# Kernel optimization log

Hardware: AMD Instinct MI355X
Metric: run time of the kernel (lower is better)

Reference implementation:

```python
import jax, jax.numpy as jnp
import numpy as np

D_MODEL = 1024
NEG_INF = -1e30


def _xavier(key, shape):
    fan_in, fan_out = shape[0], shape[1] if len(shape) > 1 else shape[0]
    limit = float(np.sqrt(6.0 / (fan_in + fan_out)))
    return jax.random.uniform(key, shape, jnp.float32, -limit, limit)


def setup_inputs() -> dict:
    key = jax.random.key(0)
    ks = jax.random.split(key, 8)
    bs, vl, ql, d = 16, 1024, 64, D_MODEL
    video_features = jax.random.normal(ks[0], (bs, vl, d), jnp.float32)
    query_features = jax.random.normal(ks[1], (bs, ql, d), jnp.float32)
    video_mask = jnp.ones((bs, vl), jnp.float32)
    query_mask = jnp.ones((bs, ql), jnp.float32)
    sim_w = _xavier(ks[2], (d, 1))
    cor_v_w = _xavier(ks[3], (1, d))
    cor_q_w = _xavier(ks[4], (1, 1))
    pool_w = _xavier(ks[5], (d, 1))          # WeightedPool weight
    mixer_w = _xavier(ks[6], (4 * d, d))     # 1x1 conv == dense mix
    mixer_b = jnp.zeros((d,), jnp.float32)
    return dict(video_features=video_features, query_features=query_features,
                video_mask=video_mask, query_mask=query_mask,
                sim_w=sim_w, cor_v_w=cor_v_w, cor_q_w=cor_q_w,
                pool_w=pool_w, mixer_w=mixer_w, mixer_b=mixer_b)


def reference(video_features, query_features, video_mask, query_mask,
              sim_w, cor_v_w, cor_q_w, pool_w, mixer_w, mixer_b):
    bs, vl, d = video_features.shape
    ql = query_features.shape[1]
    # correlation: (q_exp * v_exp).sum(-1) is just a batched matmul -> (bs, ql, vl)
    corr = jnp.einsum('bqd,bvd->bqv', query_features, video_features)
    scores = jax.nn.softmax(corr, axis=1)  # softmax over query dim (torch dim=1)
    # cor_w[b,q,d] = cor_v_w[0,d] * cor_q_w[0,0]; corr_matrix = scores^T @ cor_w
    cor_w = jnp.broadcast_to(cor_v_w * cor_q_w[0, 0], (ql, d))
    corr_matrix = jnp.einsum('bqv,qd->bvd', scores, cor_w)
    # WeightedPool over query words -> sentence feature (bs, d)
    alpha = jnp.einsum('bqd,dk->bqk', query_features, pool_w)[..., 0]  # (bs, ql)
    alpha = alpha + (1.0 - query_mask) * NEG_INF
    alphas = jax.nn.softmax(alpha, axis=1)
    sentence = jnp.einsum('bqd,bq->bd', query_features, alphas)  # (bs, d)
    # cosine similarity video vs sentence (+ masked log)
    eps = 1e-8
    dot = jnp.einsum('bvd,bd->bv', video_features, sentence)
    vn = jnp.maximum(jnp.linalg.norm(video_features, axis=-1), eps)
    sn = jnp.maximum(jnp.linalg.norm(sentence, axis=-1), eps)
    sim = dot / (vn * sn[:, None]) + jnp.log(video_mask + 1e-45)  # (bs, vl)
    # sim_features[b,v,d] = sim_w[d,0] * sim[b,v]
    sim_features = sim[..., None] * sim_w[:, 0]
    pooled_query = jnp.broadcast_to(sentence[:, None, :], (bs, vl, d))
    features = jnp.concatenate([video_features, sim_features, pooled_query, corr_matrix], axis=2)
    out = jnp.einsum('bvc,cd->bvd', features, mixer_w) + mixer_b
    return jax.nn.relu(out)
```

## Files before the change

### kernel.cpp

```cpp
#include <hip/hip_runtime.h>

#define BS 16
#define VL 1024
#define QL 64
#define DM 1024
#define MM (BS*VL)

typedef __attribute__((ext_vector_type(8))) short bf16x8;
typedef __attribute__((ext_vector_type(4))) float f32x4;

__device__ __forceinline__ unsigned short f2bf_rne(float f) {
  unsigned int u = __float_as_uint(f);
  u += 0x7fffu + ((u >> 16) & 1u);
  return (unsigned short)(u >> 16);
}
__device__ __forceinline__ void gl16(const void* g, void* l) {
  __builtin_amdgcn_global_load_lds(
      (const __attribute__((address_space(1))) unsigned int*)g,
      (__attribute__((address_space(3))) unsigned int*)l, 16, 0, 0);
}

__global__ __launch_bounds__(256) void k_sentence(
    const float* __restrict__ query, const float* __restrict__ qmask,
    const float* __restrict__ pool_w, float* __restrict__ sentence,
    float* __restrict__ sn)
{
  int b = blockIdx.x, t = threadIdx.x;
  __shared__ float alpha[QL];
  __shared__ float red[4];
  const float* qb = query + (size_t)b*QL*DM;
  {
    int q = t >> 2, part = t & 3;
    const float4* rp = (const float4*)(qb + q*DM + part*256);
    const float4* pp = (const float4*)(pool_w + part*256);
    float s = 0.f;
    for (int i = 0; i < 64; ++i) {
      float4 a = rp[i], w = pp[i];
      s += a.x*w.x + a.y*w.y + a.z*w.z + a.w*w.w;
    }
    s += __shfl_xor(s, 1);
    s += __shfl_xor(s, 2);
    if (part == 0) alpha[q] = s;
  }
  __syncthreads();
  if (t < 64) {
    float a = alpha[t] + (1.f - qmask[b*QL + t]) * (-1e30f);
    float m = a;
    for (int off = 32; off; off >>= 1) m = fmaxf(m, __shfl_xor(m, off));
    float e = expf(a - m);
    float ssum = e;
    for (int off = 32; off; off >>= 1) ssum += __shfl_xor(ssum, off);
    alpha[t] = e / ssum;
  }
  __syncthreads();
  float sq = 0.f;
  #pragma unroll
  for (int i = 0; i < 4; ++i) {
    int d = t + 256*i;
    float acc = 0.f;
    for (int q = 0; q < QL; ++q) acc += alpha[q] * qb[q*DM + d];
    sentence[(size_t)b*DM + d] = acc;
    sq += acc*acc;
  }
  for (int off = 32; off; off >>= 1) sq += __shfl_xor(sq, off);
  if ((t & 63) == 0) red[t >> 6] = sq;
  __syncthreads();
  if (t == 0) sn[b] = fmaxf(sqrtf(red[0]+red[1]+red[2]+red[3]), 1e-8f);
}

__global__ __launch_bounds__(256) void k_gemvs(
    const float* __restrict__ mixer_w, const float* __restrict__ sentence,
    const float* __restrict__ sim_w, const float* __restrict__ cor_v_w,
    const float* __restrict__ cor_q_w, float* __restrict__ partial)
{
  int d0 = blockIdx.x * 32;
  int n0 = blockIdx.y * 128;
  int t = threadIdx.x;
  int col = t & 127, kh = t >> 7;
  __shared__ float vec[18][32];
  __shared__ float red[2][18][128];
  for (int i = t; i < 18*32; i += 256) {
    int b = i >> 5, k = i & 31;
    float val;
    if (b < 16)       val = sentence[(size_t)b*DM + d0 + k];
    else if (b == 16) val = sim_w[d0 + k];
    else              val = cor_v_w[d0 + k] * cor_q_w[0];
    vec[b][k] = val;
  }
  __syncthreads();
  float acc[18];
  #pragma unroll
  for (int j = 0; j < 18; ++j) acc[j] = 0.f;
  const float* Wb = mixer_w + (size_t)(d0 + kh*16)*DM + n0 + col;
  #pragma unroll 1
  for (int k = 0; k < 16; ++k) {
    const float* wr = Wb + (size_t)k*DM;
    float w1 = wr[(size_t)1*DM*DM];
    float w2 = wr[(size_t)2*DM*DM];
    float w3 = wr[(size_t)3*DM*DM];
    int kk = kh*16 + k;
    #pragma unroll
    for (int b = 0; b < 16; ++b) acc[b] += vec[b][kk] * w2;
    acc[16] += vec[16][kk] * w1;
    acc[17] += vec[17][kk] * w3;
  }
  #pragma unroll
  for (int j = 0; j < 18; ++j) red[kh][j][col] = acc[j];
  __syncthreads();
  #pragma unroll
  for (int r = 0; r < 9; ++r) {
    int idx = t + 256*r;
    int j = idx >> 7, c2 = idx & 127;
    partial[((size_t)blockIdx.x*18 + j)*1024 + n0 + c2] = red[0][j][c2] + red[1][j][c2];
  }
}

__global__ __launch_bounds__(256) void k_reduce(
    const float* __restrict__ partial, float* __restrict__ basev,
    float* __restrict__ u_s, float* __restrict__ u_c)
{
  int idx = blockIdx.x * 256 + threadIdx.x;
  int j = idx >> 10, col = idx & 1023;
  float s = 0.f;
  #pragma unroll 4
  for (int b = 0; b < 32; ++b) s += partial[((size_t)b*18 + j)*1024 + col];
  if (j < 16)       basev[(size_t)j*1024 + col] = s;
  else if (j == 16) u_s[col] = s;
  else              u_c[col] = s;
}

__global__ __launch_bounds__(256) void k_conv(
    const float* __restrict__ video, const float* __restrict__ sentence,
    const float* __restrict__ sn, const float* __restrict__ vmask,
    const float* __restrict__ Wv,
    unsigned short* __restrict__ Ahi, unsigned short* __restrict__ Bhi,
    float* __restrict__ simv)
{
  __shared__ float tile[64][65];
  int t = threadIdx.x;
  if (blockIdx.x < 4096) {
    int wave = t >> 6, lane = t & 63;
    int row = blockIdx.x * 4 + wave;
    int b = row >> 10;
    const float4* vp = (const float4*)(video + (size_t)row*DM);
    const float4* sp = (const float4*)(sentence + (size_t)b*DM);
    float dot = 0.f, sq = 0.f;
    #pragma unroll
    for (int i = 0; i < 4; ++i) {
      float4 v = vp[lane + 64*i];
      float4 s = sp[lane + 64*i];
      dot += v.x*s.x + v.y*s.y + v.z*s.z + v.w*s.w;
      sq  += v.x*v.x + v.y*v.y + v.z*v.z + v.w*v.w;
      ushort4 h;
      h.x = f2bf_rne(v.x); h.y = f2bf_rne(v.y);
      h.z = f2bf_rne(v.z); h.w = f2bf_rne(v.w);
      *(ushort4*)(Ahi + (size_t)row*DM + (lane + 64*i)*4) = h;
    }
    #pragma unroll
    for (int off = 32; off; off >>= 1) {
      dot += __shfl_xor(dot, off);
      sq  += __shfl_xor(sq,  off);
    }
    if (lane == 0) {
      float vn = fmaxf(sqrtf(sq), 1e-8f);
      simv[row] = dot / (vn * sn[b]) + logf(vmask[row] + 1e-45f);
    }
  } else {
    int bb = blockIdx.x - 4096;
    int bk = (bb & 15) * 64;
    int bn = (bb >> 4) * 64;
    int kr = t >> 2, nc = (t & 3) * 16;
    const float4* src = (const float4*)(Wv + (size_t)(bk + kr)*DM + bn + nc);
    #pragma unroll
    for (int i = 0; i < 4; ++i) {
      float4 v = src[i];
      tile[kr][nc + i*4 + 0] = v.x;
      tile[kr][nc + i*4 + 1] = v.y;
      tile[kr][nc + i*4 + 2] = v.z;
      tile[kr][nc + i*4 + 3] = v.w;
    }
    __syncthreads();
    int n = t >> 2, kc = (t & 3) * 16;
    #pragma unroll
    for (int i = 0; i < 16; i += 4) {
      ushort4 h;
      h.x = f2bf_rne(tile[kc+i+0][n]);
      h.y = f2bf_rne(tile[kc+i+1][n]);
      h.z = f2bf_rne(tile[kc+i+2][n]);
      h.w = f2bf_rne(tile[kc+i+3][n]);
      *(ushort4*)(Bhi + (size_t)(bn+n)*DM + bk + kc + i) = h;
    }
  }
}

__global__ __launch_bounds__(256) void k_gemm(
    const unsigned short* __restrict__ Ahi, const unsigned short* __restrict__ Bhi,
    const float* __restrict__ simv, const float* __restrict__ u_s,
    const float* __restrict__ u_c, const float* __restrict__ basev,
    const float* __restrict__ mixer_b, float* __restrict__ out)
{
  __shared__ __align__(16) unsigned short At[2][128][64];
  __shared__ __align__(16) unsigned short Bt[2][128][64];

  int bid = blockIdx.x;
  int swz = (bid & 7) * 128 + (bid >> 3);
  int bm = swz >> 3;
  int bn = swz & 7;

  int t = threadIdx.x;
  int wave = t >> 6, lane = t & 63;
  int wm = (wave >> 1) * 64, wn = (wave & 1) * 64;
  int lr = lane & 15, g = lane >> 4;
  int rx = 8 * (lr & 7);

  f32x4 acc[4][4];
  #pragma unroll
  for (int i = 0; i < 4; ++i)
    #pragma unroll
    for (int j = 0; j < 4; ++j) acc[i][j] = (f32x4){0.f, 0.f, 0.f, 0.f};

  int srow = t >> 3;
  int scol = 8 * ((t & 7) ^ (srow & 7));
  const unsigned short* Ap = Ahi + (size_t)(bm*128 + srow)*DM + scol;
  const unsigned short* Bp = Bhi + (size_t)(bn*128 + srow)*DM + scol;
  char* ldsA = (char*)&At[0][0][0] + wave*1024;
  char* ldsB = (char*)&Bt[0][0][0] + wave*1024;

  #define STAGE(kt, buf) do {                                         \
    const unsigned short* _a = Ap + (kt)*64;                          \
    const unsigned short* _b = Bp + (kt)*64;                          \
    _Pragma("unroll")                                                 \
    for (int q = 0; q < 4; ++q) {                                     \
      gl16(_a + (size_t)q*32*DM, ldsA + (buf)*16384 + q*4096);        \
      gl16(_b + (size_t)q*32*DM, ldsB + (buf)*16384 + q*4096);        \
    }                                                                 \
  } while (0)

  STAGE(0, 0);
  __syncthreads();

  #pragma unroll 1
  for (int kt = 0; kt < 16; ++kt) {
    int buf = kt & 1;
    if (kt < 15) STAGE(kt + 1, buf ^ 1);
    const unsigned short* Ab = &At[buf][0][0];
    const unsigned short* Bb = &Bt[buf][0][0];
    #pragma unroll
    for (int s = 0; s < 2; ++s) {
      int cb = (s*32 + 8*g) ^ rx;
      bf16x8 af[4], bfr[4];
      #pragma unroll
      for (int mi = 0; mi < 4; ++mi)
        af[mi] = *(const bf16x8*)(Ab + (wm + mi*16 + lr)*64 + cb);
      #pragma unroll
      for (int nj = 0; nj < 4; ++nj)
        bfr[nj] = *(const bf16x8*)(Bb + (wn + nj*16 + lr)*64 + cb);
      #pragma unroll
      for (int mi = 0; mi < 4; ++mi)
        #pragma unroll
        for (int nj = 0; nj < 4; ++nj)
          acc[mi][nj] = __builtin_amdgcn_mfma_f32_16x16x32_bf16(
              af[mi], bfr[nj], acc[mi][nj], 0, 0, 0);
    }
    __syncthreads();
  }

  int orow0 = bm*128 + wm;
  int ocol0 = bn*128 + wn;
  const float* bb = basev + (size_t)((bm*128) >> 10)*DM;
  float usv[4], cv[4];
  #pragma unroll
  for (int nj = 0; nj < 4; ++nj) {
    int col = ocol0 + nj*16 + lr;
    usv[nj] = u_s[col];
    cv[nj]  = bb[col] + u_c[col] + mixer_b[col];
  }
  int rbase = g * 4;
  #pragma unroll
  for (int mi = 0; mi < 4; ++mi) {
    #pragma unroll
    for (int r = 0; r < 4; ++r) {
      int row = orow0 + mi*16 + rbase + r;
      float sim = simv[row];
      #pragma unroll
      for (int nj = 0; nj < 4; ++nj) {
        float v = acc[mi][nj][r] + sim*usv[nj] + cv[nj];
        out[(size_t)row*DM + ocol0 + nj*16 + lr] = fmaxf(v, 0.f);
      }
    }
  }
  #undef STAGE
}

extern "C" void kernel_launch(void* const* d_in, const int* in_sizes, int n_in,
                              void* d_out, int out_size, void* d_ws, size_t ws_size,
                              hipStream_t stream) {
  const float* video   = (const float*)d_in[0];
  const float* query   = (const float*)d_in[1];
  const float* vmask   = (const float*)d_in[2];
  const float* qmask   = (const float*)d_in[3];
  const float* sim_w   = (const float*)d_in[4];
  const float* cor_v_w = (const float*)d_in[5];
  const float* cor_q_w = (const float*)d_in[6];
  const float* pool_w  = (const float*)d_in[7];
  const float* mixer_w = (const float*)d_in[8];
  const float* mixer_b = (const float*)d_in[9];
  float* out = (float*)d_out;

  float* fws      = (float*)d_ws;
  float* sentence = fws;
  float* sn       = sentence + 16384;
  float* u_s      = sn + 64;
  float* u_c      = u_s + 1024;
  float* basev    = u_c + 1024;
  float* simv     = basev + 16384;
  float* partial  = simv + 16384;
  unsigned short* Ahi = (unsigned short*)(partial + 589824);
  unsigned short* Bhi = Ahi + (size_t)MM*DM;

  k_sentence<<<dim3(16), dim3(256), 0, stream>>>(query, qmask, pool_w, sentence, sn);
  k_conv<<<dim3(4352), dim3(256), 0, stream>>>(video, sentence, sn, vmask,
                                               mixer_w, Ahi, Bhi, simv);
  k_gemvs<<<dim3(32, 8), dim3(256), 0, stream>>>(mixer_w, sentence, sim_w,
                                                 cor_v_w, cor_q_w, partial);
  k_reduce<<<dim3(72), dim3(256), 0, stream>>>(partial, basev, u_s, u_c);
  k_gemm<<<dim3(1024), dim3(256), 0, stream>>>(Ahi, Bhi, simv, u_s, u_c,
                                               basev, mixer_b, out);
}
```

Measured before the change: 220.7 us.

## Enlarge GEMM tile to 256x256 with phased ping-pong schedule and parallelize sentence pooling

The main GEMM moves from 128x128 tiles with 4 waves to 256x256 tiles with 8 waves. Each k-step is split into four phases that interleave LDS fragment reads, MFMA bursts raised with s_setprio, and staggered global-to-LDS prefetches, with explicit vmcnt waits and barriers. This raises operand reuse and overlaps loads with compute. Separately, the single-block-per-batch sentence kernel is split into a 256-block alpha GEMV and a 16x8-grid pooling kernel that writes partial squared norms, which k_conv then sums. Costs are higher register pressure, 64KB of LDS, fewer GEMM blocks (256) for the available CUs, and a fragile hand-written wait/barrier schedule.

```diff
diff --git a/kernel.cpp b/kernel.cpp
--- a/kernel.cpp
+++ b/kernel.cpp
@@ -20,52 +20,64 @@
       (__attribute__((address_space(3))) unsigned int*)l, 16, 0, 0);
 }
 
-__global__ __launch_bounds__(256) void k_sentence(
+__global__ __launch_bounds__(256) void k_alpha(
+    const float* __restrict__ query, const float* __restrict__ pool_w,
+    float* __restrict__ alpha_raw)
+{
+  int wave = threadIdx.x >> 6, lane = threadIdx.x & 63;
+  int q = blockIdx.x * 4 + wave;
+  const float4* rp = (const float4*)(query + (size_t)q*DM);
+  const float4* pp = (const float4*)pool_w;
+  float s = 0.f;
+  #pragma unroll
+  for (int i = 0; i < 4; ++i) {
+    float4 a = rp[lane + 64*i], w = pp[lane + 64*i];
+    s += a.x*w.x + a.y*w.y + a.z*w.z + a.w*w.w;
+  }
+  #pragma unroll
+  for (int off = 32; off; off >>= 1) s += __shfl_xor(s, off);
+  if (lane == 0) alpha_raw[q] = s;
+}
+
+__global__ __launch_bounds__(256) void k_sentence2(
     const float* __restrict__ query, const float* __restrict__ qmask,
-    const float* __restrict__ pool_w, float* __restrict__ sentence,
-    float* __restrict__ sn)
-{
-  int b = blockIdx.x, t = threadIdx.x;
-  __shared__ float alpha[QL];
-  __shared__ float red[4];
-  const float* qb = query + (size_t)b*QL*DM;
-  {
-    int q = t >> 2, part = t & 3;
-    const float4* rp = (const float4*)(qb + q*DM + part*256);
-    const float4* pp = (const float4*)(pool_w + part*256);
-    float s = 0.f;
-    for (int i = 0; i < 64; ++i) {
-      float4 a = rp[i], w = pp[i];
-      s += a.x*w.x + a.y*w.y + a.z*w.z + a.w*w.w;
-    }
-    s += __shfl_xor(s, 1);
-    s += __shfl_xor(s, 2);
-    if (part == 0) alpha[q] = s;
-  }
-  __syncthreads();
+    const float* __restrict__ alpha_raw, float* __restrict__ sentence,
+    float* __restrict__ psq)
+{
+  int b = blockIdx.x, dc = blockIdx.y;
+  int t = threadIdx.x;
+  __shared__ float al[QL];
+  __shared__ float red2[2][128];
+  __shared__ float sqred[2];
   if (t < 64) {
-    float a = alpha[t] + (1.f - qmask[b*QL + t]) * (-1e30f);
+    float a = alpha_raw[b*QL + t] + (1.f - qmask[b*QL + t]) * (-1e30f);
     float m = a;
+    #pragma unroll
     for (int off = 32; off; off >>= 1) m = fmaxf(m, __shfl_xor(m, off));
     float e = expf(a - m);
-    float ssum = e;
-    for (int off = 32; off; off >>= 1) ssum += __shfl_xor(ssum, off);
-    alpha[t] = e / ssum;
-  }
-  __syncthreads();
-  float sq = 0.f;
-  #pragma unroll
-  for (int i = 0; i < 4; ++i) {
-    int d = t + 256*i;
-    float acc = 0.f;
-    for (int q = 0; q < QL; ++q) acc += alpha[q] * qb[q*DM + d];
-    sentence[(size_t)b*DM + d] = acc;
-    sq += acc*acc;
-  }
-  for (int off = 32; off; off >>= 1) sq += __shfl_xor(sq, off);
-  if ((t & 63) == 0) red[t >> 6] = sq;
-  __syncthreads();
-  if (t == 0) sn[b] = fmaxf(sqrtf(red[0]+red[1]+red[2]+red[3]), 1e-8f);
+    float s = e;
+    #pragma unroll
+    for (int off = 32; off; off >>= 1) s += __shfl_xor(s, off);
+    al[t] = e / s;
+  }
+  __syncthreads();
+  int col = t & 127, half = t >> 7;
+  const float* qb = query + (size_t)b*QL*DM + dc*128 + col;
+  float acc = 0.f;
+  for (int q = half*32; q < half*32 + 32; ++q)
+    acc += al[q] * qb[(size_t)q*DM];
+  red2[half][col] = acc;
+  __syncthreads();
+  if (t < 128) {
+    float s = red2[0][t] + red2[1][t];
+    sentence[(size_t)b*DM + dc*128 + t] = s;
+    float sq = s*s;
+    #pragma unroll
+    for (int off = 32; off; off >>= 1) sq += __shfl_xor(sq, off);
+    if ((t & 63) == 0) sqred[t >> 6] = sq;
+  }
+  __syncthreads();
+  if (t == 0) psq[b*8 + dc] = sqred[0] + sqred[1];
 }
 
 __global__ __launch_bounds__(256) void k_gemvs(
@@ -131,7 +143,7 @@
 
 __global__ __launch_bounds__(256) void k_conv(
     const float* __restrict__ video, const float* __restrict__ sentence,
-    const float* __restrict__ sn, const float* __restrict__ vmask,
+    const float* __restrict__ psq, const float* __restrict__ vmask,
     const float* __restrict__ Wv,
     unsigned short* __restrict__ Ahi, unsigned short* __restrict__ Bhi,
     float* __restrict__ simv)
@@ -162,8 +174,12 @@
       sq  += __shfl_xor(sq,  off);
     }
     if (lane == 0) {
-      float vn = fmaxf(sqrtf(sq), 1e-8f);
-      simv[row] = dot / (vn * sn[b]) + logf(vmask[row] + 1e-45f);
+      float ss = 0.f;
+      #pragma unroll
+      for (int i = 0; i < 8; ++i) ss += psq[b*8 + i];
+      float snv = fmaxf(sqrtf(ss), 1e-8f);
+      float vn  = fmaxf(sqrtf(sq), 1e-8f);
+      simv[row] = dot / (vn * snv) + logf(vmask[row] + 1e-45f);
     }
   } else {
     int bb = blockIdx.x - 4096;
@@ -193,81 +209,117 @@
   }
 }
 
-__global__ __launch_bounds__(256) void k_gemm(
+__global__ __launch_bounds__(512, 2) void k_gemm(
     const unsigned short* __restrict__ Ahi, const unsigned short* __restrict__ Bhi,
     const float* __restrict__ simv, const float* __restrict__ u_s,
     const float* __restrict__ u_c, const float* __restrict__ basev,
     const float* __restrict__ mixer_b, float* __restrict__ out)
 {
-  __shared__ __align__(16) unsigned short At[2][128][64];
-  __shared__ __align__(16) unsigned short Bt[2][128][64];
+  __shared__ __align__(16) unsigned short A_lds[2][256][64];
+  __shared__ __align__(16) unsigned short B_lds[2][256][64];
 
   int bid = blockIdx.x;
-  int swz = (bid & 7) * 128 + (bid >> 3);
-  int bm = swz >> 3;
-  int bn = swz & 7;
+  int swz = (bid & 7) * 32 + (bid >> 3);
+  int bm = swz >> 2;
+  int bn = swz & 3;
 
   int t = threadIdx.x;
-  int wave = t >> 6, lane = t & 63;
-  int wm = (wave >> 1) * 64, wn = (wave & 1) * 64;
+  int w = t >> 6, lane = t & 63;
+  int wmh = w >> 2;
+  int wq  = w & 3;
   int lr = lane & 15, g = lane >> 4;
   int rx = 8 * (lr & 7);
 
-  f32x4 acc[4][4];
-  #pragma unroll
-  for (int i = 0; i < 4; ++i)
+  int rsub = lane >> 3, cch = lane & 7;
+  int csw = 8 * (cch ^ rsub);
+  const unsigned short* Asrc =
+      Ahi + (size_t)(bm*256 + wmh*128 + wq*32 + rsub)*DM + csw;
+  const unsigned short* Bsrc =
+      Bhi + (size_t)(bn*256 + wq*64 + wmh*32 + rsub)*DM + csw;
+
+  f32x4 acc[8][4];
+  #pragma unroll
+  for (int i = 0; i < 8; ++i)
     #pragma unroll
     for (int j = 0; j < 4; ++j) acc[i][j] = (f32x4){0.f, 0.f, 0.f, 0.f};
 
-  int srow = t >> 3;
-  int scol = 8 * ((t & 7) ^ (srow & 7));
-  const unsigned short* Ap = Ahi + (size_t)(bm*128 + srow)*DM + scol;
-  const unsigned short* Bp = Bhi + (size_t)(bn*128 + srow)*DM + scol;
-  char* ldsA = (char*)&At[0][0][0] + wave*1024;
-  char* ldsB = (char*)&Bt[0][0][0] + wave*1024;
-
-  #define STAGE(kt, buf) do {                                         \
-    const unsigned short* _a = Ap + (kt)*64;                          \
-    const unsigned short* _b = Bp + (kt)*64;                          \
-    _Pragma("unroll")                                                 \
-    for (int q = 0; q < 4; ++q) {                                     \
-      gl16(_a + (size_t)q*32*DM, ldsA + (buf)*16384 + q*4096);        \
-      gl16(_b + (size_t)q*32*DM, ldsB + (buf)*16384 + q*4096);        \
-    }                                                                 \
-  } while (0)
-
-  STAGE(0, 0);
-  __syncthreads();
+  bf16x8 a_frag[8];
+  bf16x8 b_frag[4];
+
+#define PH_READS_A(h)                                                      \
+  _Pragma("unroll") for (int m = 0; m < 4; ++m)                            \
+    _Pragma("unroll") for (int ks = 0; ks < 2; ++ks)                       \
+      a_frag[m*2+ks] = *(const bf16x8*)                                    \
+          &A_lds[buf][wmh*128 + ((h)*4+m)*16 + lr][(ks*32 + 8*g) ^ rx];
+
+#define PH_READS_B(v)                                                      \
+  _Pragma("unroll") for (int n = 0; n < 2; ++n)                            \
+    _Pragma("unroll") for (int ks = 0; ks < 2; ++ks)                       \
+      b_frag[n*2+ks] = *(const bf16x8*)                                    \
+          &B_lds[buf][wq*64 + ((v)*2+n)*16 + lr][(ks*32 + 8*g) ^ rx];
+
+#define PH_MFMA(h, v)                                                      \
+  __builtin_amdgcn_s_setprio(1);                                           \
+  _Pragma("unroll") for (int m = 0; m < 4; ++m)                            \
+    _Pragma("unroll") for (int n = 0; n < 2; ++n)                          \
+      _Pragma("unroll") for (int ks = 0; ks < 2; ++ks)                     \
+        acc[(h)*4+m][(v)*2+n] = __builtin_amdgcn_mfma_f32_16x16x32_bf16(   \
+            a_frag[m*2+ks], b_frag[n*2+ks], acc[(h)*4+m][(v)*2+n], 0,0,0); \
+  __builtin_amdgcn_s_setprio(0);
+
+  {
+    unsigned short* Ad = &A_lds[0][wmh*128 + wq*32][0];
+    unsigned short* Bd = &B_lds[0][wq*64 + wmh*32][0];
+    #pragma unroll
+    for (int j = 0; j < 4; ++j) {
+      gl16(Asrc + (size_t)j*8*DM, Ad + j*8*64);
+      gl16(Bsrc + (size_t)j*8*DM, Bd + j*8*64);
+    }
+  }
 
   #pragma unroll 1
   for (int kt = 0; kt < 16; ++kt) {
     int buf = kt & 1;
-    if (kt < 15) STAGE(kt + 1, buf ^ 1);
-    const unsigned short* Ab = &At[buf][0][0];
-    const unsigned short* Bb = &Bt[buf][0][0];
-    #pragma unroll
-    for (int s = 0; s < 2; ++s) {
-      int cb = (s*32 + 8*g) ^ rx;
-      bf16x8 af[4], bfr[4];
-      #pragma unroll
-      for (int mi = 0; mi < 4; ++mi)
-        af[mi] = *(const bf16x8*)(Ab + (wm + mi*16 + lr)*64 + cb);
-      #pragma unroll
-      for (int nj = 0; nj < 4; ++nj)
-        bfr[nj] = *(const bf16x8*)(Bb + (wn + nj*16 + lr)*64 + cb);
-      #pragma unroll
-      for (int mi = 0; mi < 4; ++mi)
-        #pragma unroll
-        for (int nj = 0; nj < 4; ++nj)
-          acc[mi][nj] = __builtin_amdgcn_mfma_f32_16x16x32_bf16(
-              af[mi], bfr[nj], acc[mi][nj], 0, 0, 0);
-    }
-    __syncthreads();
-  }
-
-  int orow0 = bm*128 + wm;
-  int ocol0 = bn*128 + wn;
-  const float* bb = basev + (size_t)((bm*128) >> 10)*DM;
+    const unsigned short* An = Asrc + (kt+1)*64;
+    const unsigned short* Bn = Bsrc + (kt+1)*64;
+    unsigned short* Ad = &A_lds[buf^1][wmh*128 + wq*32][0];
+    unsigned short* Bd = &B_lds[buf^1][wq*64 + wmh*32][0];
+    bool pf = kt < 15;
+
+    if (pf) { gl16(An, Ad); gl16(An + (size_t)8*DM, Ad + 8*64); }
+    if (pf) asm volatile("s_waitcnt vmcnt(2)" ::: "memory");
+    else    asm volatile("s_waitcnt vmcnt(0)" ::: "memory");
+    __builtin_amdgcn_sched_barrier(0);
+    __builtin_amdgcn_s_barrier();
+    PH_READS_A(0)
+    PH_READS_B(0)
+    __builtin_amdgcn_s_barrier();
+    PH_MFMA(0, 0)
+    __builtin_amdgcn_s_barrier();
+
+    if (pf) { gl16(An + (size_t)16*DM, Ad + 16*64); gl16(An + (size_t)24*DM, Ad + 24*64); }
+    PH_READS_B(1)
+    __builtin_amdgcn_s_barrier();
+    PH_MFMA(0, 1)
+    __builtin_amdgcn_s_barrier();
+
+    if (pf) { gl16(Bn, Bd); gl16(Bn + (size_t)8*DM, Bd + 8*64); }
+    PH_READS_A(1)
+    PH_READS_B(0)
+    __builtin_amdgcn_s_barrier();
+    PH_MFMA(1, 0)
+    __builtin_amdgcn_s_barrier();
+
+    if (pf) { gl16(Bn + (size_t)16*DM, Bd + 16*64); gl16(Bn + (size_t)24*DM, Bd + 24*64); }
+    PH_READS_B(1)
+    __builtin_amdgcn_s_barrier();
+    PH_MFMA(1, 1)
+    __builtin_amdgcn_s_barrier();
+  }
+
+  int orow0 = bm*256 + wmh*128;
+  int ocol0 = bn*256 + wq*64;
+  const float* bb = basev + (size_t)(bm >> 2)*DM;
   float usv[4], cv[4];
   #pragma unroll
   for (int nj = 0; nj < 4; ++nj) {
@@ -277,7 +329,7 @@
   }
   int rbase = g * 4;
   #pragma unroll
-  for (int mi = 0; mi < 4; ++mi) {
+  for (int mi = 0; mi < 8; ++mi) {
     #pragma unroll
     for (int r = 0; r < 4; ++r) {
       int row = orow0 + mi*16 + rbase + r;
@@ -289,7 +341,9 @@
       }
     }
   }
-  #undef STAGE
+#undef PH_READS_A
+#undef PH_READS_B
+#undef PH_MFMA
 }
 
 extern "C" void kernel_launch(void* const* d_in, const int* in_sizes, int n_in,
@@ -307,23 +361,26 @@
   const float* mixer_b = (const float*)d_in[9];
   float* out = (float*)d_out;
 
-  float* fws      = (float*)d_ws;
-  float* sentence = fws;
-  float* sn       = sentence + 16384;
-  float* u_s      = sn + 64;
-  float* u_c      = u_s + 1024;
-  float* basev    = u_c + 1024;
-  float* simv     = basev + 16384;
-  float* partial  = simv + 16384;
+  float* fws       = (float*)d_ws;
+  float* sentence  = fws;
+  float* u_s       = sentence + 16384;
+  float* u_c       = u_s + 1024;
+  float* basev     = u_c + 1024;
+  float* simv      = basev + 16384;
+  float* alpha_raw = simv + 16384;
+  float* psq       = alpha_raw + 1024;
+  float* partial   = psq + 128;
   unsigned short* Ahi = (unsigned short*)(partial + 589824);
   unsigned short* Bhi = Ahi + (size_t)MM*DM;
 
-  k_sentence<<<dim3(16), dim3(256), 0, stream>>>(query, qmask, pool_w, sentence, sn);
-  k_conv<<<dim3(4352), dim3(256), 0, stream>>>(video, sentence, sn, vmask,
+  k_alpha<<<dim3(256), dim3(256), 0, stream>>>(query, pool_w, alpha_raw);
+  k_sentence2<<<dim3(16, 8), dim3(256), 0, stream>>>(query, qmask, alpha_raw,
+                                                     sentence, psq);
+  k_conv<<<dim3(4352), dim3(256), 0, stream>>>(video, sentence, psq, vmask,
                                                mixer_w, Ahi, Bhi, simv);
   k_gemvs<<<dim3(32, 8), dim3(256), 0, stream>>>(mixer_w, sentence, sim_w,
                                                  cor_v_w, cor_q_w, partial);
   k_reduce<<<dim3(72), dim3(256), 0, stream>>>(partial, basev, u_s, u_c);
-  k_gemm<<<dim3(1024), dim3(256), 0, stream>>>(Ahi, Bhi, simv, u_s, u_c,
-                                               basev, mixer_b, out);
-}
+  k_gemm<<<dim3(256), dim3(512), 0, stream>>>(Ahi, Bhi, simv, u_s, u_c,
+                                              basev, mixer_b, out);
+}
```

Result: no change. 219.4 us (-0.6%).

## Split sentence kernel across columns and fold partial reduction into GEMM prologue

Applied to the files above, without the earlier changes.

The sentence-pooling kernel now runs on a 16x8 grid, each block handling 128 feature columns and writing partial squared norms. The conv kernel sums these partials to get the sentence norm. The separate reduce kernel is removed: each GEMM block sums the 32 k-chunk partials for its batch and column tile into shared memory while its first stage load is in flight. This drops one launch and parallelises the small serial front kernel, but every GEMM block now repeats reduction loads that were done once before.

```diff
diff --git a/kernel.cpp b/kernel.cpp
--- a/kernel.cpp
+++ b/kernel.cpp
@@ -20,14 +20,15 @@
       (__attribute__((address_space(3))) unsigned int*)l, 16, 0, 0);
 }
 
-__global__ __launch_bounds__(256) void k_sentence(
+__global__ __launch_bounds__(256) void k_sent(
     const float* __restrict__ query, const float* __restrict__ qmask,
     const float* __restrict__ pool_w, float* __restrict__ sentence,
-    float* __restrict__ sn)
+    float* __restrict__ psq)
 {
-  int b = blockIdx.x, t = threadIdx.x;
-  __shared__ float alpha[QL];
-  __shared__ float red[4];
+  int b = blockIdx.x, dc = blockIdx.y, t = threadIdx.x;
+  __shared__ float al[QL];
+  __shared__ float red2[2][128];
+  __shared__ float sqred[2];
   const float* qb = query + (size_t)b*QL*DM;
   {
     int q = t >> 2, part = t & 3;
@@ -40,32 +41,38 @@
     }
     s += __shfl_xor(s, 1);
     s += __shfl_xor(s, 2);
-    if (part == 0) alpha[q] = s;
+    if (part == 0) al[q] = s;
   }
   __syncthreads();
   if (t < 64) {
-    float a = alpha[t] + (1.f - qmask[b*QL + t]) * (-1e30f);
+    float a = al[t] + (1.f - qmask[b*QL + t]) * (-1e30f);
     float m = a;
+    #pragma unroll
     for (int off = 32; off; off >>= 1) m = fmaxf(m, __shfl_xor(m, off));
     float e = expf(a - m);
     float ssum = e;
+    #pragma unroll
     for (int off = 32; off; off >>= 1) ssum += __shfl_xor(ssum, off);
-    alpha[t] = e / ssum;
-  }
-  __syncthreads();
-  float sq = 0.f;
-  #pragma unroll
-  for (int i = 0; i < 4; ++i) {
-    int d = t + 256*i;
-    float acc = 0.f;
-    for (int q = 0; q < QL; ++q) acc += alpha[q] * qb[q*DM + d];
-    sentence[(size_t)b*DM + d] = acc;
-    sq += acc*acc;
-  }
-  for (int off = 32; off; off >>= 1) sq += __shfl_xor(sq, off);
-  if ((t & 63) == 0) red[t >> 6] = sq;
-  __syncthreads();
-  if (t == 0) sn[b] = fmaxf(sqrtf(red[0]+red[1]+red[2]+red[3]), 1e-8f);
+    al[t] = e / ssum;
+  }
+  __syncthreads();
+  int col = t & 127, half = t >> 7;
+  const float* qp = qb + dc*128 + col;
+  float acc = 0.f;
+  for (int q = half*32; q < half*32 + 32; ++q)
+    acc += al[q] * qp[(size_t)q*DM];
+  red2[half][col] = acc;
+  __syncthreads();
+  if (t < 128) {
+    float s = red2[0][t] + red2[1][t];
+    sentence[(size_t)b*DM + dc*128 + t] = s;
+    float sq = s*s;
+    #pragma unroll
+    for (int off = 32; off; off >>= 1) sq += __shfl_xor(sq, off);
+    if ((t & 63) == 0) sqred[t >> 6] = sq;
+  }
+  __syncthreads();
+  if (t == 0) psq[b*8 + dc] = sqred[0] + sqred[1];
 }
 
 __global__ __launch_bounds__(256) void k_gemvs(
@@ -115,23 +122,9 @@
   }
 }
 
-__global__ __launch_bounds__(256) void k_reduce(
-    const float* __restrict__ partial, float* __restrict__ basev,
-    float* __restrict__ u_s, float* __restrict__ u_c)
-{
-  int idx = blockIdx.x * 256 + threadIdx.x;
-  int j = idx >> 10, col = idx & 1023;
-  float s = 0.f;
-  #pragma unroll 4
-  for (int b = 0; b < 32; ++b) s += partial[((size_t)b*18 + j)*1024 + col];
-  if (j < 16)       basev[(size_t)j*1024 + col] = s;
-  else if (j == 16) u_s[col] = s;
-  else              u_c[col] = s;
-}
-
 __global__ __launch_bounds__(256) void k_conv(
     const float* __restrict__ video, const float* __restrict__ sentence,
-    const float* __restrict__ sn, const float* __restrict__ vmask,
+    const float* __restrict__ psq, const float* __restrict__ vmask,
     const float* __restrict__ Wv,
     unsigned short* __restrict__ Ahi, unsigned short* __restrict__ Bhi,
     float* __restrict__ simv)
@@ -162,8 +155,12 @@
       sq  += __shfl_xor(sq,  off);
     }
     if (lane == 0) {
-      float vn = fmaxf(sqrtf(sq), 1e-8f);
-      simv[row] = dot / (vn * sn[b]) + logf(vmask[row] + 1e-45f);
+      float ss = 0.f;
+      #pragma unroll
+      for (int i = 0; i < 8; ++i) ss += psq[b*8 + i];
+      float snv = fmaxf(sqrtf(ss), 1e-8f);
+      float vn  = fmaxf(sqrtf(sq), 1e-8f);
+      simv[row] = dot / (vn * snv) + logf(vmask[row] + 1e-45f);
     }
   } else {
     int bb = blockIdx.x - 4096;
@@ -195,17 +192,18 @@
 
 __global__ __launch_bounds__(256) void k_gemm(
     const unsigned short* __restrict__ Ahi, const unsigned short* __restrict__ Bhi,
-    const float* __restrict__ simv, const float* __restrict__ u_s,
-    const float* __restrict__ u_c, const float* __restrict__ basev,
+    const float* __restrict__ simv, const float* __restrict__ partial,
     const float* __restrict__ mixer_b, float* __restrict__ out)
 {
   __shared__ __align__(16) unsigned short At[2][128][64];
   __shared__ __align__(16) unsigned short Bt[2][128][64];
+  __shared__ float bL[128], uL[128], cL[128];
 
   int bid = blockIdx.x;
   int swz = (bid & 7) * 128 + (bid >> 3);
   int bm = swz >> 3;
   int bn = swz & 7;
+  int batch = bm >> 3;
 
   int t = threadIdx.x;
   int wave = t >> 6, lane = t & 63;
@@ -237,6 +235,26 @@
   } while (0)
 
   STAGE(0, 0);
+
+  {
+    int nbase = bn * 128;
+    if (t < 128) {
+      float s = 0.f;
+      #pragma unroll 4
+      for (int kc = 0; kc < 32; ++kc)
+        s += partial[((size_t)kc*18 + batch)*1024 + nbase + t];
+      bL[t] = s;
+    } else {
+      int c = t - 128;
+      float s16 = 0.f, s17 = 0.f;
+      #pragma unroll 4
+      for (int kc = 0; kc < 32; ++kc) {
+        s16 += partial[((size_t)kc*18 + 16)*1024 + nbase + c];
+        s17 += partial[((size_t)kc*18 + 17)*1024 + nbase + c];
+      }
+      uL[c] = s16; cL[c] = s17;
+    }
+  }
   __syncthreads();
 
   #pragma unroll 1
@@ -267,13 +285,12 @@
 
   int orow0 = bm*128 + wm;
   int ocol0 = bn*128 + wn;
-  const float* bb = basev + (size_t)((bm*128) >> 10)*DM;
   float usv[4], cv[4];
   #pragma unroll
   for (int nj = 0; nj < 4; ++nj) {
-    int col = ocol0 + nj*16 + lr;
-    usv[nj] = u_s[col];
-    cv[nj]  = bb[col] + u_c[col] + mixer_b[col];
+    int lc = wn + nj*16 + lr;
+    usv[nj] = uL[lc];
+    cv[nj]  = bL[lc] + cL[lc] + mixer_b[ocol0 + nj*16 + lr];
   }
   int rbase = g * 4;
   #pragma unroll
@@ -309,21 +326,18 @@
 
   float* fws      = (float*)d_ws;
   float* sentence = fws;
-  float* sn       = sentence + 16384;
-  float* u_s      = sn + 64;
-  float* u_c      = u_s + 1024;
-  float* basev    = u_c + 1024;
-  float* simv     = basev + 16384;
+  float* psq      = sentence + 16384;
+  float* simv     = psq + 128;
   float* partial  = simv + 16384;
   unsigned short* Ahi = (unsigned short*)(partial + 589824);
   unsigned short* Bhi = Ahi + (size_t)MM*DM;
 
-  k_sentence<<<dim3(16), dim3(256), 0, stream>>>(query, qmask, pool_w, sentence, sn);
-  k_conv<<<dim3(4352), dim3(256), 0, stream>>>(video, sentence, sn, vmask,
-                                               mixer_w, Ahi, Bhi, simv);
+  k_sent<<<dim3(16, 8), dim3(256), 0, stream>>>(query, qmask, pool_w,
+                                                sentence, psq);
   k_gemvs<<<dim3(32, 8), dim3(256), 0, stream>>>(mixer_w, sentence, sim_w,
                                                  cor_v_w, cor_q_w, partial);
-  k_reduce<<<dim3(72), dim3(256), 0, stream>>>(partial, basev, u_s, u_c);
-  k_gemm<<<dim3(1024), dim3(256), 0, stream>>>(Ahi, Bhi, simv, u_s, u_c,
-                                               basev, mixer_b, out);
-}
+  k_conv<<<dim3(4352), dim3(256), 0, stream>>>(video, sentence, psq, vmask,
+                                               mixer_w, Ahi, Bhi, simv);
+  k_gemm<<<dim3(1024), dim3(256), 0, stream>>>(Ahi, Bhi, simv, partial,
+                                               mixer_b, out);
+}
```

After: 222.1 us. Within noise of the previous version (+0.6%).
